# Performance work log

Measured on AMD Instinct MI355X. Metric: run time of the kernel, lower is better.

Reference implementation:

```python
import jax, jax.numpy as jnp
import numpy as np

B, N, D = 32, 20, 64          # graph pairs, max node set size, node state dim
NODE_F, EDGE_F = 16, 8        # raw feature dims
E_PER, PROP = 40, 5           # edges per graph, propagation steps
NC2 = N * (N - 1) // 2        # 190
TEMP, ITERS = 0.1, 20         # sinkhorn temperature / iterations
SRC, DST = np.triu_indices(N, 1)   # source_list / destination_list (len NC2)


def _lin(k, fin, fout):
    return jax.random.normal(k, (fin, fout), dtype=jnp.float32) / np.sqrt(fin).astype(np.float32)


def setup_inputs():
    key = jax.random.key(0)
    ks = jax.random.split(key, 24)
    tn, te = 2 * B * N, 2 * B * E_PER
    gid = jnp.repeat(jnp.arange(2 * B), E_PER)   # edges stay within their graph
    inp = {
        'node_features': jax.random.normal(ks[0], (tn, NODE_F), jnp.float32),
        'edge_features': jax.random.normal(ks[1], (te, EDGE_F), jnp.float32),
        'query_adj': (jax.random.uniform(ks[2], (B, N, N)) < 0.3).astype(jnp.float32),
        'corpus_adj': (jax.random.uniform(ks[3], (B, N, N)) < 0.3).astype(jnp.float32),
        'from_idx': jax.random.randint(ks[4], (te,), 0, N) + gid * N,
        'to_idx': jax.random.randint(ks[5], (te,), 0, N) + gid * N,
    }
    # GraphEncoder
    inp['Wn'] = _lin(ks[6], NODE_F, D); inp['bn'] = jnp.zeros(D)
    inp['We'] = _lin(ks[7], EDGE_F, D); inp['be'] = jnp.zeros(D)
    # GraphPropLayer: message net (in 3D) and node-update net (in 2D)
    inp['Wm1'] = _lin(ks[8], 3 * D, D); inp['bm1'] = jnp.zeros(D)
    inp['Wm2'] = _lin(ks[9], D, D);     inp['bm2'] = jnp.zeros(D)
    inp['Wu1'] = _lin(ks[10], 2 * D, D); inp['bu1'] = jnp.zeros(D)
    inp['Wu2'] = _lin(ks[11], D, D);     inp['bu2'] = jnp.zeros(D)
    # node_sinkhorn_feature_layers: Linear(D,N) -> ReLU -> Linear(N,N)
    inp['Ws1'] = _lin(ks[12], D, N); inp['bs1'] = jnp.zeros(N)
    inp['Ws2'] = _lin(ks[13], N, N); inp['bs2'] = jnp.zeros(N)
    # lrl_network: Linear(2D+1, D) -> ReLU -> Linear(D, D)
    inp['Wl1'] = _lin(ks[14], 2 * D + 1, D); inp['bl1'] = jnp.zeros(D)
    inp['Wl2'] = _lin(ks[15], D, D);         inp['bl2'] = jnp.zeros(D)
    return inp


def _mlp2(x, W1, b1, W2, b2):
    return jax.nn.relu(x @ W1 + b1) @ W2 + b2


def _sinkhorn(log_alpha):
    la = log_alpha / TEMP
    for _ in range(ITERS):
        la = la - jax.nn.logsumexp(la, axis=2, keepdims=True)
        la = la - jax.nn.logsumexp(la, axis=1, keepdims=True)
    return jnp.exp(la)


def _nc2_edge_emb(H, adj, Wl1, bl1, Wl2, bl2):
    s, d = H[:, SRC], H[:, DST]          # [B, NC2, D]
    e = adj[:, SRC, DST][..., None]      # [B, NC2, 1]
    fwd = _mlp2(jnp.concatenate([s, d, e], -1), Wl1, bl1, Wl2, bl2)
    bwd = _mlp2(jnp.concatenate([d, s, e], -1), Wl1, bl1, Wl2, bl2)
    return fwd + bwd


def reference(node_features, edge_features, query_adj, corpus_adj, from_idx, to_idx,
              Wn, bn, We, be, Wm1, bm1, Wm2, bm2, Wu1, bu1, Wu2, bu2,
              Ws1, bs1, Ws2, bs2, Wl1, bl1, Wl2, bl2):
    # encoder
    h = node_features @ Wn + bn
    e = edge_features @ We + be
    # GMN-style gather -> MLP -> scatter propagation
    for _ in range(PROP):
        msg = _mlp2(jnp.concatenate([h[from_idx], h[to_idx], e], -1), Wm1, bm1, Wm2, bm2)
        agg = jax.ops.segment_sum(msg, to_idx, num_segments=2 * B * N)
        h = _mlp2(jnp.concatenate([h, agg], -1), Wu1, bu1, Wu2, bu2)
    # split_and_stack (all graphs have exactly N nodes): query even, corpus odd
    H = h.reshape(2 * B, N, D)
    Hq, Hc = H[0::2], H[1::2]
    # node Sinkhorn over L1 cdist of transformed features
    Tq = _mlp2(Hq, Ws1, bs1, Ws2, bs2)
    Tc = _mlp2(Hc, Ws1, bs1, Ws2, bs2)
    cost = jnp.abs(Tq[:, :, None, :] - Tc[:, None, :, :]).sum(-1)   # [B, N, N]
    P = _sinkhorn(-cost)                                            # node transport plan
    qe = _nc2_edge_emb(Hq, query_adj, Wl1, bl1, Wl2, bl2)           # [B, NC2, D]
    ce = _nc2_edge_emb(Hc, corpus_adj, Wl1, bl1, Wl2, bl2)
    # 4-way gather-multiply edge scores: [B, NC2, NC2]
    straight = P[:, SRC[:, None], SRC[None, :]] * P[:, DST[:, None], DST[None, :]]
    cross = P[:, SRC[:, None], DST[None, :]] * P[:, DST[:, None], SRC[None, :]]
    esi = jnp.maximum(straight, cross)                              # use_max=True
    eplan = _sinkhorn(jnp.log(esi + 1e-6))                          # use_second_sinkhorn_log
    # use_m_ms_edge=True: pairwise asymmetric L1 alignment distance
    diff = qe[:, :, None, :] - ce[:, None, :, :]                    # [B, NC2, NC2, D]
    dist = (eplan * (jax.nn.relu(diff).sum(-1) + jax.nn.relu(-diff).sum(-1))).sum((-1, -2))
    return dist                                                      # [B]
```

## Files before the change

kernel.cpp:

```cpp
#include <hip/hip_runtime.h>
#include <math.h>

#define B_     32
#define N_     20
#define D_     64
#define NODE_F 16
#define EDGE_F 8
#define E_PER  40
#define PROP   5
#define NC2    190
#define ITERS  20
#define INV_TEMP 10.0f
#define TN (2*B_*N_)
#define TE (2*B_*E_PER)
#define NG (2*B_)

struct PairTab { int s[NC2]; int d[NC2]; };
constexpr PairTab make_pairs() {
    PairTab t{};
    int idx = 0;
    for (int i = 0; i < N_; ++i)
        for (int j = i + 1; j < N_; ++j) { t.s[idx] = i; t.d[idx] = j; ++idx; }
    return t;
}
__device__ constexpr PairTab PAIRS = make_pairs();

__device__ __forceinline__ float rlane(float x, int k) {
#if __has_builtin(__builtin_amdgcn_readlane)
    return __int_as_float(__builtin_amdgcn_readlane(__float_as_int(x), k));
#else
    return __shfl(x, k, 64);
#endif
}

template<int CTRL>
__device__ __forceinline__ float dppmov(float x) {
    return __int_as_float(__builtin_amdgcn_update_dpp(
        0, __float_as_int(x), CTRL, 0xf, 0xf, false));
}
__device__ __forceinline__ float rowsum16(float x) {
    x += dppmov<0x121>(x);
    x += dppmov<0x122>(x);
    x += dppmov<0x124>(x);
    x += dppmov<0x128>(x);
    return x;
}
__device__ __forceinline__ float rowmax16(float x) {
    x = fmaxf(x, dppmov<0x121>(x));
    x = fmaxf(x, dppmov<0x122>(x));
    x = fmaxf(x, dppmov<0x124>(x));
    x = fmaxf(x, dppmov<0x128>(x));
    return x;
}
__device__ __forceinline__ float nrcp(float x) {
    float r = __builtin_amdgcn_rcpf(x);
    r = r * fmaf(-x, r, 2.0f);
    return r;
}

__global__ __launch_bounds__(256) void k_encode(
    const float* __restrict__ nf, const float* __restrict__ ef,
    const float* __restrict__ Wn, const float* __restrict__ bn,
    const float* __restrict__ We, const float* __restrict__ be,
    float* __restrict__ h, float* __restrict__ eemb, float* __restrict__ agg)
{
    int gid = blockIdx.x * 256 + threadIdx.x;
    int f = gid & 63, r = gid >> 6;
    if (r < TN) {
        float acc = bn[f];
#pragma unroll
        for (int k = 0; k < NODE_F; ++k) acc += nf[r * NODE_F + k] * Wn[k * D_ + f];
        h[r * D_ + f] = acc;
        agg[r * D_ + f] = 0.f;
    } else if (r < TN + TE) {
        int r2 = r - TN;
        float acc = be[f];
#pragma unroll
        for (int k = 0; k < EDGE_F; ++k) acc += ef[r2 * EDGE_F + k] * We[k * D_ + f];
        eemb[r2 * D_ + f] = acc;
    }
}

#define EPW 4
__global__ __launch_bounds__(256) void k_msg(
    const float* __restrict__ h, const float* __restrict__ eemb,
    const int* __restrict__ fidx, const int* __restrict__ tidx,
    const float* __restrict__ Wm1, const float* __restrict__ bm1,
    const float* __restrict__ Wm2, const float* __restrict__ bm2,
    float* __restrict__ agg)
{
    int wid = (blockIdx.x * 256 + threadIdx.x) >> 6;
    int f = threadIdx.x & 63;
    int ebase = wid * EPW;
    float xf[EPW], xt[EPW], xe[EPW];
    int to[EPW];
#pragma unroll
    for (int s = 0; s < EPW; ++s) {
        int e = ebase + s;
        int fr = fidx[e]; to[s] = tidx[e];
        xf[s] = h[fr * D_ + f];
        xt[s] = h[to[s] * D_ + f];
        xe[s] = eemb[e * D_ + f];
    }
    float b1 = bm1[f];
    float acc[EPW];
#pragma unroll
    for (int s = 0; s < EPW; ++s) acc[s] = b1;
#pragma unroll 4
    for (int k = 0; k < D_; ++k) {
        float w0 = Wm1[k * D_ + f];
        float w1 = Wm1[(D_ + k) * D_ + f];
        float w2 = Wm1[(2 * D_ + k) * D_ + f];
#pragma unroll
        for (int s = 0; s < EPW; ++s)
            acc[s] += rlane(xf[s], k) * w0 + rlane(xt[s], k) * w1 + rlane(xe[s], k) * w2;
    }
    float b2 = bm2[f];
    float out[EPW];
#pragma unroll
    for (int s = 0; s < EPW; ++s) { acc[s] = fmaxf(acc[s], 0.f); out[s] = b2; }
#pragma unroll 4
    for (int k = 0; k < D_; ++k) {
        float w = Wm2[k * D_ + f];
#pragma unroll
        for (int s = 0; s < EPW; ++s) out[s] += rlane(acc[s], k) * w;
    }
#pragma unroll
    for (int s = 0; s < EPW; ++s) atomicAdd(&agg[to[s] * D_ + f], out[s]);
}

#define NPW 2
__global__ __launch_bounds__(256) void k_update(
    float* __restrict__ h, float* __restrict__ agg,
    const float* __restrict__ Wu1, const float* __restrict__ bu1,
    const float* __restrict__ Wu2, const float* __restrict__ bu2)
{
    int wid = (blockIdx.x * 256 + threadIdx.x) >> 6;
    int f = threadIdx.x & 63;
    int nbase = wid * NPW;
    float xh[NPW], xa[NPW];
#pragma unroll
    for (int s = 0; s < NPW; ++s) {
        xh[s] = h[(nbase + s) * D_ + f];
        xa[s] = agg[(nbase + s) * D_ + f];
    }
    float b1 = bu1[f];
    float acc[NPW];
#pragma unroll
    for (int s = 0; s < NPW; ++s) acc[s] = b1;
#pragma unroll 4
    for (int k = 0; k < D_; ++k) {
        float w0 = Wu1[k * D_ + f];
        float w1 = Wu1[(D_ + k) * D_ + f];
#pragma unroll
        for (int s = 0; s < NPW; ++s)
            acc[s] += rlane(xh[s], k) * w0 + rlane(xa[s], k) * w1;
    }
    float b2 = bu2[f];
    float out[NPW];
#pragma unroll
    for (int s = 0; s < NPW; ++s) { acc[s] = fmaxf(acc[s], 0.f); out[s] = b2; }
#pragma unroll 4
    for (int k = 0; k < D_; ++k) {
        float w = Wu2[k * D_ + f];
#pragma unroll
        for (int s = 0; s < NPW; ++s) out[s] += rlane(acc[s], k) * w;
    }
#pragma unroll
    for (int s = 0; s < NPW; ++s) {
        h[(nbase + s) * D_ + f] = out[s];
        agg[(nbase + s) * D_ + f] = 0.f;
    }
}

#define PPW 4
__global__ __launch_bounds__(256) void k_edge(
    const float* __restrict__ h,
    const float* __restrict__ qadj, const float* __restrict__ cadj,
    const float* __restrict__ Wl1, const float* __restrict__ bl1,
    const float* __restrict__ Wl2, const float* __restrict__ bl2,
    float* __restrict__ emb)
{
    int wid = (blockIdx.x * 256 + threadIdx.x) >> 6;
    int f = threadIdx.x & 63;
    int base = wid * PPW;
    float sv[PPW], dv[PPW], av[PPW];
#pragma unroll
    for (int s = 0; s < PPW; ++s) {
        int slot = base + s;
        int g = slot / NC2, p = slot - g * NC2;
        int sp = PAIRS.s[p], dp = PAIRS.d[p];
        sv[s] = h[(g * N_ + sp) * D_ + f];
        dv[s] = h[(g * N_ + dp) * D_ + f];
        const float* adj = (g & 1) ? cadj : qadj;
        av[s] = adj[(g >> 1) * N_ * N_ + sp * N_ + dp];
    }
    float b1 = bl1[f];
    float w128 = Wl1[128 * D_ + f];
    float aF[PPW], aB[PPW];
#pragma unroll
    for (int s = 0; s < PPW; ++s) { float t0 = b1 + av[s] * w128; aF[s] = t0; aB[s] = t0; }
#pragma unroll 2
    for (int k = 0; k < D_; ++k) {
        float w0 = Wl1[k * D_ + f];
        float w1 = Wl1[(D_ + k) * D_ + f];
#pragma unroll
        for (int s = 0; s < PPW; ++s) {
            float a = rlane(sv[s], k), c = rlane(dv[s], k);
            aF[s] += a * w0 + c * w1;
            aB[s] += c * w0 + a * w1;
        }
    }
    float b2 = 2.f * bl2[f];
    float hs[PPW], out[PPW];
#pragma unroll
    for (int s = 0; s < PPW; ++s) {
        hs[s] = fmaxf(aF[s], 0.f) + fmaxf(aB[s], 0.f);
        out[s] = b2;
    }
#pragma unroll 4
    for (int k = 0; k < D_; ++k) {
        float w = Wl2[k * D_ + f];
#pragma unroll
        for (int s = 0; s < PPW; ++s) out[s] += rlane(hs[s], k) * w;
    }
#pragma unroll
    for (int s = 0; s < PPW; ++s) emb[(size_t)(base + s) * D_ + f] = out[s];
}

__global__ __launch_bounds__(1024) void k_simsink(
    const float* __restrict__ h,
    const float* __restrict__ Ws1, const float* __restrict__ bs1,
    const float* __restrict__ Ws2, const float* __restrict__ bs2,
    float* __restrict__ eplan, float* __restrict__ dout)
{
    __shared__ float sH[2][N_][D_];
    __shared__ float sA[2][N_][N_];
    __shared__ float sT[2][N_][N_];
    __shared__ float sLa[N_][N_];
    __shared__ float sU20[N_], sV20[N_];
    __shared__ float sP[N_][N_];
    __shared__ float colbuf[64][200];
    __shared__ float sInvC[192];
    __shared__ short sQs[192], sQd[192];
    int b = blockIdx.x, t = threadIdx.x;

    for (int idx = t; idx < 2 * N_ * D_; idx += 1024) {
        int s = idx / (N_ * D_), rem = idx % (N_ * D_), i = rem / D_, f = rem % D_;
        sH[s][i][f] = h[((2 * b + s) * N_ + i) * D_ + f];
    }
    __syncthreads();
    for (int idx = t; idx < 2 * N_ * N_; idx += 1024) {
        int s = idx / (N_ * N_), rem = idx % (N_ * N_), i = rem / N_, k = rem % N_;
        float a = bs1[k];
        for (int ff = 0; ff < D_; ++ff) a += sH[s][i][ff] * Ws1[ff * N_ + k];
        sA[s][i][k] = fmaxf(a, 0.f);
    }
    __syncthreads();
    for (int idx = t; idx < 2 * N_ * N_; idx += 1024) {
        int s = idx / (N_ * N_), rem = idx % (N_ * N_), i = rem / N_, k = rem % N_;
        float a = bs2[k];
        for (int j = 0; j < N_; ++j) a += sA[s][i][j] * Ws2[j * N_ + k];
        sT[s][i][k] = a;
    }
    __syncthreads();
    for (int idx = t; idx < N_ * N_; idx += 1024) {
        int i = idx / N_, j = idx % N_;
        float c = 0.f;
        for (int k = 0; k < N_; ++k) c += fabsf(sT[0][i][k] - sT[1][j][k]);
        sLa[i][j] = -c * INV_TEMP;
    }
    if (t < N_) sV20[t] = 0.f;
    __syncthreads();
    for (int it = 0; it < ITERS; ++it) {
        if (t < N_) {
            float m = -1e30f;
            for (int q = 0; q < N_; ++q) m = fmaxf(m, sLa[t][q] - sV20[q]);
            float ss = 0.f;
            for (int q = 0; q < N_; ++q) ss += __expf(sLa[t][q] - sV20[q] - m);
            sU20[t] = m + __logf(ss);
        }
        __syncthreads();
        if (t < N_) {
            float m = -1e30f;
            for (int p = 0; p < N_; ++p) m = fmaxf(m, sLa[p][t] - sU20[p]);
            float ss = 0.f;
            for (int p = 0; p < N_; ++p) ss += __expf(sLa[p][t] - sU20[p] - m);
            sV20[t] = m + __logf(ss);
        }
        __syncthreads();
    }
    if (t < N_ * N_) {
        int i = t / N_, j = t % N_;
        sP[i][j] = __expf(sLa[i][j] - sU20[i] - sV20[j]);
    }
    if (t < 192) {
        int tt = t < NC2 ? t : NC2 - 1;
        sQs[t] = (short)PAIRS.s[tt];
        sQd[t] = (short)PAIRS.d[tt];
    }
    if (t == 0) dout[b] = 0.f;
    __syncthreads();

    int w = t >> 6, l = t & 63, g = l >> 4, l16 = l & 15;
    int rslot = w * 4 + g;

    int sp[3], dp[3];
    bool pv[3];
#pragma unroll
    for (int i = 0; i < 3; ++i) {
        int p = rslot + 64 * i;
        pv[i] = (p < NC2);
        int pp = pv[i] ? p : 0;
        sp[i] = sQs[pp]; dp[i] = sQd[pp];
    }
    int sq[12], dq[12];
    bool qv[12];
#pragma unroll
    for (int j = 0; j < 12; ++j) {
        int q = l16 + 16 * j;
        qv[j] = (q < NC2);
        int qq = qv[j] ? q : 0;
        sq[j] = sQs[qq]; dq[j] = sQd[qq];
    }

    float E[3][12];
#pragma unroll
    for (int i = 0; i < 3; ++i) {
        float mi = 1e-30f;
#pragma unroll
        for (int j = 0; j < 12; ++j) {
            float x = 0.f;
            if (pv[i] && qv[j]) {
                float st = sP[sp[i]][sq[j]] * sP[dp[i]][dq[j]];
                float cr = sP[sp[i]][dq[j]] * sP[dp[i]][sq[j]];
                x = fmaxf(st, cr) + 1e-6f;
            }
            E[i][j] = x;
            mi = fmaxf(mi, x);
        }
        mi = rowmax16(mi);
        float invm = nrcp(mi);
#pragma unroll
        for (int j = 0; j < 12; ++j) {
            float r = E[i][j] * invm;
            float r2 = r * r, r4 = r2 * r2, r8 = r4 * r4;
            E[i][j] = r8 * r2;
        }
    }

    float invS[3];
    for (int it = 0; it < ITERS; ++it) {
#pragma unroll
        for (int i = 0; i < 3; ++i) {
            float s01 = E[i][0] + E[i][1], s23 = E[i][2] + E[i][3];
            float s45 = E[i][4] + E[i][5], s67 = E[i][6] + E[i][7];
            float s89 = E[i][8] + E[i][9], sab = E[i][10] + E[i][11];
            float S = ((s01 + s23) + (s45 + s67)) + (s89 + sab);
            S = rowsum16(S);
            invS[i] = nrcp(fmaxf(S, 1e-30f));
        }
#pragma unroll
        for (int j = 0; j < 12; ++j) {
            float pc = E[0][j] * invS[0];
            pc = fmaf(E[1][j], invS[1], pc);
            pc = fmaf(E[2][j], invS[2], pc);
            colbuf[rslot][l16 + 16 * j] = pc;
        }
        __syncthreads();
        if (t < 192) {
            float a0 = 0.f, a1 = 0.f, a2 = 0.f, a3 = 0.f;
#pragma unroll
            for (int s = 0; s < 16; ++s) {
                a0 += colbuf[4 * s + 0][t];
                a1 += colbuf[4 * s + 1][t];
                a2 += colbuf[4 * s + 2][t];
                a3 += colbuf[4 * s + 3][t];
            }
            float c = (a0 + a1) + (a2 + a3);
            sInvC[t] = nrcp(fmaxf(c, 1e-30f));
        }
        __syncthreads();
        float ic[12];
#pragma unroll
        for (int j = 0; j < 12; ++j) ic[j] = sInvC[l16 + 16 * j];
#pragma unroll
        for (int i = 0; i < 3; ++i) {
#pragma unroll
            for (int j = 0; j < 12; ++j) {
                float tmp = E[i][j] * invS[i];
                E[i][j] = tmp * ic[j];
            }
        }
    }

    float* ep = eplan + (size_t)b * NC2 * NC2;
#pragma unroll
    for (int i = 0; i < 3; ++i) {
        if (pv[i]) {
            int p = rslot + 64 * i;
            float* row = ep + (size_t)p * NC2;
#pragma unroll
            for (int j = 0; j < 12; ++j) {
                if (qv[j]) row[l16 + 16 * j] = E[i][j];
            }
        }
    }
}

__global__ __launch_bounds__(256) void k_dist(
    const float* __restrict__ emb, const float* __restrict__ eplan, float* __restrict__ dout)
{
    int b = blockIdx.x, c = blockIdx.y;
    int w = threadIdx.x >> 6, l = threadIdx.x & 63;
    const float* qe = emb + (size_t)(2 * b) * NC2 * D_;
    const float* ce = emb + (size_t)(2 * b + 1) * NC2 * D_;
    const float* W = eplan + (size_t)b * NC2 * NC2;
    float acc = 0.f;
    int pbase = c * 16 + w * 4;
    for (int i = 0; i < 4; ++i) {
        int p = pbase + i;
        if (p >= NC2) break;
        float qv = qe[(size_t)p * D_ + l];
        const float* wrow = W + (size_t)p * NC2;
        for (int q = 0; q < NC2; ++q)
            acc += wrow[q] * fabsf(qv - ce[(size_t)q * D_ + l]);
    }
#pragma unroll
    for (int off = 32; off; off >>= 1) acc += __shfl_xor(acc, off);
    if (l == 0) atomicAdd(&dout[b], acc);
}

extern "C" void kernel_launch(void* const* d_in, const int* in_sizes, int n_in,
                              void* d_out, int out_size, void* d_ws, size_t ws_size,
                              hipStream_t stream)
{
    const float* nf   = (const float*)d_in[0];
    const float* ef   = (const float*)d_in[1];
    const float* qadj = (const float*)d_in[2];
    const float* cadj = (const float*)d_in[3];
    const int*   fidx = (const int*)d_in[4];
    const int*   tidx = (const int*)d_in[5];
    const float* Wn  = (const float*)d_in[6];  const float* bn  = (const float*)d_in[7];
    const float* We  = (const float*)d_in[8];  const float* be  = (const float*)d_in[9];
    const float* Wm1 = (const float*)d_in[10]; const float* bm1 = (const float*)d_in[11];
    const float* Wm2 = (const float*)d_in[12]; const float* bm2 = (const float*)d_in[13];
    const float* Wu1 = (const float*)d_in[14]; const float* bu1 = (const float*)d_in[15];
    const float* Wu2 = (const float*)d_in[16]; const float* bu2 = (const float*)d_in[17];
    const float* Ws1 = (const float*)d_in[18]; const float* bs1 = (const float*)d_in[19];
    const float* Ws2 = (const float*)d_in[20]; const float* bs2 = (const float*)d_in[21];
    const float* Wl1 = (const float*)d_in[22]; const float* bl1 = (const float*)d_in[23];
    const float* Wl2 = (const float*)d_in[24]; const float* bl2 = (const float*)d_in[25];

    float* ws    = (float*)d_ws;
    float* h     = ws;
    float* agg   = h    + (size_t)TN * D_;
    float* eemb  = agg  + (size_t)TN * D_;
    float* emb   = eemb + (size_t)TE * D_;
    float* eplan = emb  + (size_t)NG * NC2 * D_;
    float* dout  = (float*)d_out;

    k_encode<<<(TN + TE) * D_ / 256, 256, 0, stream>>>(nf, ef, Wn, bn, We, be, h, eemb, agg);
    for (int s = 0; s < PROP; ++s) {
        k_msg<<<TE / EPW / 4, 256, 0, stream>>>(h, eemb, fidx, tidx, Wm1, bm1, Wm2, bm2, agg);
        k_update<<<TN / NPW / 4, 256, 0, stream>>>(h, agg, Wu1, bu1, Wu2, bu2);
    }
    k_simsink<<<B_, 1024, 0, stream>>>(h, Ws1, bs1, Ws2, bs2, eplan, dout);
    k_edge<<<NG * NC2 / PPW / 4, 256, 0, stream>>>(h, qadj, cadj, Wl1, bl1, Wl2, bl2, emb);
    k_dist<<<dim3(B_, 12), 256, 0, stream>>>(emb, eplan, dout);
}
```

Before: 315.0 us.

## Fuse encoder, propagation, sinkhorn and edge embedding into one per-pair megakernel

Replaces the encode, five msg/update rounds, node/edge sinkhorn and edge-embedding kernels with a single 1024-thread block per graph pair. Node states, edge embeddings and aggregates live in shared memory, so the intermediate global round-trips and roughly a dozen launches go away. The node sinkhorn now runs on one wavefront using shuffles. The edge sinkhorn's first iteration is done in log domain instead of the max-normalised power trick. The cost is that only 32 blocks run all the propagation and edge-MLP work, which leaves most of the GPU idle during those phases.

```diff
diff --git a/kernel.cpp b/kernel.cpp
--- a/kernel.cpp
+++ b/kernel.cpp
@@ -26,30 +26,21 @@
 __device__ constexpr PairTab PAIRS = make_pairs();
 
 __device__ __forceinline__ float rlane(float x, int k) {
-#if __has_builtin(__builtin_amdgcn_readlane)
     return __int_as_float(__builtin_amdgcn_readlane(__float_as_int(x), k));
-#else
-    return __shfl(x, k, 64);
-#endif
-}
-
+}
 template<int CTRL>
 __device__ __forceinline__ float dppmov(float x) {
     return __int_as_float(__builtin_amdgcn_update_dpp(
         0, __float_as_int(x), CTRL, 0xf, 0xf, false));
 }
 __device__ __forceinline__ float rowsum16(float x) {
-    x += dppmov<0x121>(x);
-    x += dppmov<0x122>(x);
-    x += dppmov<0x124>(x);
-    x += dppmov<0x128>(x);
+    x += dppmov<0x121>(x); x += dppmov<0x122>(x);
+    x += dppmov<0x124>(x); x += dppmov<0x128>(x);
     return x;
 }
 __device__ __forceinline__ float rowmax16(float x) {
-    x = fmaxf(x, dppmov<0x121>(x));
-    x = fmaxf(x, dppmov<0x122>(x));
-    x = fmaxf(x, dppmov<0x124>(x));
-    x = fmaxf(x, dppmov<0x128>(x));
+    x = fmaxf(x, dppmov<0x121>(x)); x = fmaxf(x, dppmov<0x122>(x));
+    x = fmaxf(x, dppmov<0x124>(x)); x = fmaxf(x, dppmov<0x128>(x));
     return x;
 }
 __device__ __forceinline__ float nrcp(float x) {
@@ -58,351 +49,406 @@
     return r;
 }
 
-__global__ __launch_bounds__(256) void k_encode(
+__global__ __launch_bounds__(1024) void k_mega(
     const float* __restrict__ nf, const float* __restrict__ ef,
+    const float* __restrict__ qadj, const float* __restrict__ cadj,
+    const int* __restrict__ fidx, const int* __restrict__ tidx,
     const float* __restrict__ Wn, const float* __restrict__ bn,
     const float* __restrict__ We, const float* __restrict__ be,
-    float* __restrict__ h, float* __restrict__ eemb, float* __restrict__ agg)
-{
-    int gid = blockIdx.x * 256 + threadIdx.x;
-    int f = gid & 63, r = gid >> 6;
-    if (r < TN) {
-        float acc = bn[f];
-#pragma unroll
-        for (int k = 0; k < NODE_F; ++k) acc += nf[r * NODE_F + k] * Wn[k * D_ + f];
-        h[r * D_ + f] = acc;
-        agg[r * D_ + f] = 0.f;
-    } else if (r < TN + TE) {
-        int r2 = r - TN;
-        float acc = be[f];
-#pragma unroll
-        for (int k = 0; k < EDGE_F; ++k) acc += ef[r2 * EDGE_F + k] * We[k * D_ + f];
-        eemb[r2 * D_ + f] = acc;
-    }
-}
-
-#define EPW 4
-__global__ __launch_bounds__(256) void k_msg(
-    const float* __restrict__ h, const float* __restrict__ eemb,
-    const int* __restrict__ fidx, const int* __restrict__ tidx,
     const float* __restrict__ Wm1, const float* __restrict__ bm1,
     const float* __restrict__ Wm2, const float* __restrict__ bm2,
-    float* __restrict__ agg)
-{
-    int wid = (blockIdx.x * 256 + threadIdx.x) >> 6;
-    int f = threadIdx.x & 63;
-    int ebase = wid * EPW;
-    float xf[EPW], xt[EPW], xe[EPW];
-    int to[EPW];
-#pragma unroll
-    for (int s = 0; s < EPW; ++s) {
-        int e = ebase + s;
-        int fr = fidx[e]; to[s] = tidx[e];
-        xf[s] = h[fr * D_ + f];
-        xt[s] = h[to[s] * D_ + f];
-        xe[s] = eemb[e * D_ + f];
-    }
-    float b1 = bm1[f];
-    float acc[EPW];
-#pragma unroll
-    for (int s = 0; s < EPW; ++s) acc[s] = b1;
-#pragma unroll 4
-    for (int k = 0; k < D_; ++k) {
-        float w0 = Wm1[k * D_ + f];
-        float w1 = Wm1[(D_ + k) * D_ + f];
-        float w2 = Wm1[(2 * D_ + k) * D_ + f];
-#pragma unroll
-        for (int s = 0; s < EPW; ++s)
-            acc[s] += rlane(xf[s], k) * w0 + rlane(xt[s], k) * w1 + rlane(xe[s], k) * w2;
-    }
-    float b2 = bm2[f];
-    float out[EPW];
-#pragma unroll
-    for (int s = 0; s < EPW; ++s) { acc[s] = fmaxf(acc[s], 0.f); out[s] = b2; }
-#pragma unroll 4
-    for (int k = 0; k < D_; ++k) {
-        float w = Wm2[k * D_ + f];
-#pragma unroll
-        for (int s = 0; s < EPW; ++s) out[s] += rlane(acc[s], k) * w;
-    }
-#pragma unroll
-    for (int s = 0; s < EPW; ++s) atomicAdd(&agg[to[s] * D_ + f], out[s]);
-}
-
-#define NPW 2
-__global__ __launch_bounds__(256) void k_update(
-    float* __restrict__ h, float* __restrict__ agg,
     const float* __restrict__ Wu1, const float* __restrict__ bu1,
-    const float* __restrict__ Wu2, const float* __restrict__ bu2)
-{
-    int wid = (blockIdx.x * 256 + threadIdx.x) >> 6;
-    int f = threadIdx.x & 63;
-    int nbase = wid * NPW;
-    float xh[NPW], xa[NPW];
-#pragma unroll
-    for (int s = 0; s < NPW; ++s) {
-        xh[s] = h[(nbase + s) * D_ + f];
-        xa[s] = agg[(nbase + s) * D_ + f];
-    }
-    float b1 = bu1[f];
-    float acc[NPW];
-#pragma unroll
-    for (int s = 0; s < NPW; ++s) acc[s] = b1;
-#pragma unroll 4
-    for (int k = 0; k < D_; ++k) {
-        float w0 = Wu1[k * D_ + f];
-        float w1 = Wu1[(D_ + k) * D_ + f];
-#pragma unroll
-        for (int s = 0; s < NPW; ++s)
-            acc[s] += rlane(xh[s], k) * w0 + rlane(xa[s], k) * w1;
-    }
-    float b2 = bu2[f];
-    float out[NPW];
-#pragma unroll
-    for (int s = 0; s < NPW; ++s) { acc[s] = fmaxf(acc[s], 0.f); out[s] = b2; }
-#pragma unroll 4
-    for (int k = 0; k < D_; ++k) {
-        float w = Wu2[k * D_ + f];
-#pragma unroll
-        for (int s = 0; s < NPW; ++s) out[s] += rlane(acc[s], k) * w;
-    }
-#pragma unroll
-    for (int s = 0; s < NPW; ++s) {
-        h[(nbase + s) * D_ + f] = out[s];
-        agg[(nbase + s) * D_ + f] = 0.f;
-    }
-}
-
-#define PPW 4
-__global__ __launch_bounds__(256) void k_edge(
-    const float* __restrict__ h,
-    const float* __restrict__ qadj, const float* __restrict__ cadj,
+    const float* __restrict__ Wu2, const float* __restrict__ bu2,
+    const float* __restrict__ Ws1, const float* __restrict__ bs1,
+    const float* __restrict__ Ws2, const float* __restrict__ bs2,
     const float* __restrict__ Wl1, const float* __restrict__ bl1,
     const float* __restrict__ Wl2, const float* __restrict__ bl2,
-    float* __restrict__ emb)
+    float* __restrict__ emb, float* __restrict__ eplan, float* __restrict__ dout)
 {
-    int wid = (blockIdx.x * 256 + threadIdx.x) >> 6;
-    int f = threadIdx.x & 63;
-    int base = wid * PPW;
-    float sv[PPW], dv[PPW], av[PPW];
-#pragma unroll
-    for (int s = 0; s < PPW; ++s) {
-        int slot = base + s;
-        int g = slot / NC2, p = slot - g * NC2;
-        int sp = PAIRS.s[p], dp = PAIRS.d[p];
-        sv[s] = h[(g * N_ + sp) * D_ + f];
-        dv[s] = h[(g * N_ + dp) * D_ + f];
-        const float* adj = (g & 1) ? cadj : qadj;
-        av[s] = adj[(g >> 1) * N_ * N_ + sp * N_ + dp];
-    }
-    float b1 = bl1[f];
-    float w128 = Wl1[128 * D_ + f];
-    float aF[PPW], aB[PPW];
-#pragma unroll
-    for (int s = 0; s < PPW; ++s) { float t0 = b1 + av[s] * w128; aF[s] = t0; aB[s] = t0; }
-#pragma unroll 2
-    for (int k = 0; k < D_; ++k) {
-        float w0 = Wl1[k * D_ + f];
-        float w1 = Wl1[(D_ + k) * D_ + f];
-#pragma unroll
-        for (int s = 0; s < PPW; ++s) {
-            float a = rlane(sv[s], k), c = rlane(dv[s], k);
-            aF[s] += a * w0 + c * w1;
-            aB[s] += c * w0 + a * w1;
-        }
-    }
-    float b2 = 2.f * bl2[f];
-    float hs[PPW], out[PPW];
-#pragma unroll
-    for (int s = 0; s < PPW; ++s) {
-        hs[s] = fmaxf(aF[s], 0.f) + fmaxf(aB[s], 0.f);
-        out[s] = b2;
-    }
-#pragma unroll 4
-    for (int k = 0; k < D_; ++k) {
-        float w = Wl2[k * D_ + f];
-#pragma unroll
-        for (int s = 0; s < PPW; ++s) out[s] += rlane(hs[s], k) * w;
-    }
-#pragma unroll
-    for (int s = 0; s < PPW; ++s) emb[(size_t)(base + s) * D_ + f] = out[s];
-}
-
-__global__ __launch_bounds__(1024) void k_simsink(
-    const float* __restrict__ h,
-    const float* __restrict__ Ws1, const float* __restrict__ bs1,
-    const float* __restrict__ Ws2, const float* __restrict__ bs2,
-    float* __restrict__ eplan, float* __restrict__ dout)
-{
-    __shared__ float sH[2][N_][D_];
-    __shared__ float sA[2][N_][N_];
-    __shared__ float sT[2][N_][N_];
-    __shared__ float sLa[N_][N_];
-    __shared__ float sU20[N_], sV20[N_];
+    __shared__ float sh_h[40][64];
+    __shared__ short sFr[80], sTo[80];
+    __shared__ short sQs[192], sQd[192];
     __shared__ float sP[N_][N_];
-    __shared__ float colbuf[64][200];
-    __shared__ float sInvC[192];
-    __shared__ short sQs[192], sQd[192];
-    int b = blockIdx.x, t = threadIdx.x;
-
-    for (int idx = t; idx < 2 * N_ * D_; idx += 1024) {
-        int s = idx / (N_ * D_), rem = idx % (N_ * D_), i = rem / D_, f = rem % D_;
-        sH[s][i][f] = h[((2 * b + s) * N_ + i) * D_ + f];
-    }
-    __syncthreads();
-    for (int idx = t; idx < 2 * N_ * N_; idx += 1024) {
-        int s = idx / (N_ * N_), rem = idx % (N_ * N_), i = rem / N_, k = rem % N_;
-        float a = bs1[k];
-        for (int ff = 0; ff < D_; ++ff) a += sH[s][i][ff] * Ws1[ff * N_ + k];
-        sA[s][i][k] = fmaxf(a, 0.f);
-    }
-    __syncthreads();
-    for (int idx = t; idx < 2 * N_ * N_; idx += 1024) {
-        int s = idx / (N_ * N_), rem = idx % (N_ * N_), i = rem / N_, k = rem % N_;
-        float a = bs2[k];
-        for (int j = 0; j < N_; ++j) a += sA[s][i][j] * Ws2[j * N_ + k];
-        sT[s][i][k] = a;
-    }
-    __syncthreads();
-    for (int idx = t; idx < N_ * N_; idx += 1024) {
-        int i = idx / N_, j = idx % N_;
-        float c = 0.f;
-        for (int k = 0; k < N_; ++k) c += fabsf(sT[0][i][k] - sT[1][j][k]);
-        sLa[i][j] = -c * INV_TEMP;
-    }
-    if (t < N_) sV20[t] = 0.f;
-    __syncthreads();
-    for (int it = 0; it < ITERS; ++it) {
-        if (t < N_) {
-            float m = -1e30f;
-            for (int q = 0; q < N_; ++q) m = fmaxf(m, sLa[t][q] - sV20[q]);
-            float ss = 0.f;
-            for (int q = 0; q < N_; ++q) ss += __expf(sLa[t][q] - sV20[q] - m);
-            sU20[t] = m + __logf(ss);
-        }
-        __syncthreads();
-        if (t < N_) {
-            float m = -1e30f;
-            for (int p = 0; p < N_; ++p) m = fmaxf(m, sLa[p][t] - sU20[p]);
-            float ss = 0.f;
-            for (int p = 0; p < N_; ++p) ss += __expf(sLa[p][t] - sU20[p] - m);
-            sV20[t] = m + __logf(ss);
-        }
-        __syncthreads();
-    }
-    if (t < N_ * N_) {
-        int i = t / N_, j = t % N_;
-        sP[i][j] = __expf(sLa[i][j] - sU20[i] - sV20[j]);
+    __shared__ float sVbuf[192];
+    __shared__ float region[12416];
+    float* eemb = region;
+    float* agg  = region + 80 * 64;
+    float* sT   = region;
+    float* sLa  = region + 800;
+    float* colbuf = region;
+
+    int b = blockIdx.x, t = threadIdx.x, w = t >> 6, l = t & 63;
+
+    if (t < 80) {
+        sFr[t] = (short)(fidx[b * 80 + t] - b * 40);
+        sTo[t] = (short)(tidx[b * 80 + t] - b * 40);
     }
     if (t < 192) {
         int tt = t < NC2 ? t : NC2 - 1;
-        sQs[t] = (short)PAIRS.s[tt];
-        sQd[t] = (short)PAIRS.d[tt];
+        sQs[t] = (short)PAIRS.s[tt]; sQd[t] = (short)PAIRS.d[tt];
     }
     if (t == 0) dout[b] = 0.f;
+#pragma unroll
+    for (int s = 0; s < 3; ++s) {
+        int r = w + 16 * s;
+        if (r < 40) {
+            float acc = bn[l];
+#pragma unroll
+            for (int k = 0; k < NODE_F; ++k) acc += nf[(b * 40 + r) * NODE_F + k] * Wn[k * 64 + l];
+            sh_h[r][l] = acc;
+        }
+    }
+#pragma unroll
+    for (int s = 0; s < 5; ++s) {
+        int e = w * 5 + s;
+        float acc = be[l];
+#pragma unroll
+        for (int k = 0; k < EDGE_F; ++k) acc += ef[(b * 80 + e) * EDGE_F + k] * We[k * 64 + l];
+        eemb[e * 64 + l] = acc;
+    }
+    for (int idx = t; idx < 2560; idx += 1024) agg[idx] = 0.f;
     __syncthreads();
 
-    int w = t >> 6, l = t & 63, g = l >> 4, l16 = l & 15;
-    int rslot = w * 4 + g;
-
-    int sp[3], dp[3];
-    bool pv[3];
-#pragma unroll
-    for (int i = 0; i < 3; ++i) {
-        int p = rslot + 64 * i;
-        pv[i] = (p < NC2);
-        int pp = pv[i] ? p : 0;
-        sp[i] = sQs[pp]; dp[i] = sQd[pp];
-    }
-    int sq[12], dq[12];
-    bool qv[12];
-#pragma unroll
-    for (int j = 0; j < 12; ++j) {
-        int q = l16 + 16 * j;
-        qv[j] = (q < NC2);
-        int qq = qv[j] ? q : 0;
-        sq[j] = sQs[qq]; dq[j] = sQd[qq];
-    }
-
-    float E[3][12];
-#pragma unroll
-    for (int i = 0; i < 3; ++i) {
-        float mi = 1e-30f;
+    for (int step = 0; step < PROP; ++step) {
+        int eb = w * 5;
+        float xf[5], xt[5], xe[5]; int dst[5];
+#pragma unroll
+        for (int s = 0; s < 5; ++s) {
+            int fr = sFr[eb + s]; dst[s] = sTo[eb + s];
+            xf[s] = sh_h[fr][l];
+            xt[s] = sh_h[dst[s]][l];
+            xe[s] = eemb[(eb + s) * 64 + l];
+        }
+        float b1 = bm1[l];
+        float acc[5];
+#pragma unroll
+        for (int s = 0; s < 5; ++s) acc[s] = b1;
+#pragma unroll 4
+        for (int k = 0; k < 64; ++k) {
+            float w0 = Wm1[k * 64 + l];
+            float w1 = Wm1[(64 + k) * 64 + l];
+            float w2 = Wm1[(128 + k) * 64 + l];
+#pragma unroll
+            for (int s = 0; s < 5; ++s)
+                acc[s] += rlane(xf[s], k) * w0 + rlane(xt[s], k) * w1 + rlane(xe[s], k) * w2;
+        }
+        float b2 = bm2[l];
+        float out[5];
+#pragma unroll
+        for (int s = 0; s < 5; ++s) { acc[s] = fmaxf(acc[s], 0.f); out[s] = b2; }
+#pragma unroll 4
+        for (int k = 0; k < 64; ++k) {
+            float ww = Wm2[k * 64 + l];
+#pragma unroll
+            for (int s = 0; s < 5; ++s) out[s] += rlane(acc[s], k) * ww;
+        }
+#pragma unroll
+        for (int s = 0; s < 5; ++s) atomicAdd(&agg[dst[s] * 64 + l], out[s]);
+        __syncthreads();
+
+        float xh[3], xa[3];
+        bool nv[3] = {true, true, (w < 8)};
+#pragma unroll
+        for (int s = 0; s < 3; ++s) {
+            int r = w + 16 * s;
+            if (nv[s]) { xh[s] = sh_h[r][l]; xa[s] = agg[r * 64 + l]; }
+            else { xh[s] = 0.f; xa[s] = 0.f; }
+        }
+        float c1 = bu1[l];
+        float a2[3];
+#pragma unroll
+        for (int s = 0; s < 3; ++s) a2[s] = c1;
+#pragma unroll 4
+        for (int k = 0; k < 64; ++k) {
+            float wa = Wu1[k * 64 + l];
+            float wb = Wu1[(64 + k) * 64 + l];
+#pragma unroll
+            for (int s = 0; s < 3; ++s)
+                a2[s] += rlane(xh[s], k) * wa + rlane(xa[s], k) * wb;
+        }
+        float c2 = bu2[l];
+        float o2[3];
+#pragma unroll
+        for (int s = 0; s < 3; ++s) { a2[s] = fmaxf(a2[s], 0.f); o2[s] = c2; }
+#pragma unroll 4
+        for (int k = 0; k < 64; ++k) {
+            float ww = Wu2[k * 64 + l];
+#pragma unroll
+            for (int s = 0; s < 3; ++s) o2[s] += rlane(a2[s], k) * ww;
+        }
+#pragma unroll
+        for (int s = 0; s < 3; ++s) {
+            int r = w + 16 * s;
+            if (nv[s]) { sh_h[r][l] = o2[s]; agg[r * 64 + l] = 0.f; }
+        }
+        __syncthreads();
+    }
+
+    {
+        int lk = (l < 20) ? l : 0;
+#pragma unroll
+        for (int s = 0; s < 3; ++s) {
+            int r = w + 16 * s;
+            if (r < 40) {
+                float hv = sh_h[r][l];
+                float a = bs1[lk];
+#pragma unroll 4
+                for (int ff = 0; ff < 64; ++ff) a += rlane(hv, ff) * Ws1[ff * 20 + lk];
+                a = fmaxf(a, 0.f);
+                float t2 = bs2[lk];
+#pragma unroll
+                for (int j = 0; j < 20; ++j) t2 += rlane(a, j) * Ws2[j * 20 + lk];
+                if (l < 20) sT[(r >= 20) * 400 + (r % 20) * 20 + l] = t2;
+            }
+        }
+    }
+    __syncthreads();
+    if (t < 400) {
+        int i = t / 20, j = t % 20;
+        float c = 0.f;
+#pragma unroll
+        for (int k = 0; k < 20; ++k) c += fabsf(sT[i * 20 + k] - sT[400 + j * 20 + k]);
+        sLa[i * 20 + j] = -c * INV_TEMP;
+    }
+    __syncthreads();
+
+    if (w == 0) {
+        int q = l & 31, r2 = l >> 5;
+        bool qok = (q < 20);
+        float A20[10], u10[10];
+#pragma unroll
+        for (int i = 0; i < 10; ++i) {
+            int r = 2 * i + r2;
+            A20[i] = qok ? sLa[r * 20 + q] : -1e30f;
+        }
+        float vq = 0.f;
+        for (int it = 0; it < ITERS; ++it) {
+#pragma unroll
+            for (int i = 0; i < 10; ++i) {
+                float x = A20[i] - vq;
+                float m = x;
+#pragma unroll
+                for (int off = 16; off; off >>= 1) m = fmaxf(m, __shfl_xor(m, off));
+                float s = __expf(x - m);
+#pragma unroll
+                for (int off = 16; off; off >>= 1) s += __shfl_xor(s, off);
+                u10[i] = m + __logf(s);
+            }
+            float pm = -1e30f;
+#pragma unroll
+            for (int i = 0; i < 10; ++i) pm = fmaxf(pm, A20[i] - u10[i]);
+            float ps = 0.f;
+#pragma unroll
+            for (int i = 0; i < 10; ++i) ps += __expf(A20[i] - u10[i] - pm);
+            float om = __shfl_xor(pm, 32), os = __shfl_xor(ps, 32);
+            float M = fmaxf(pm, om);
+            float S = ps * __expf(pm - M) + os * __expf(om - M);
+            vq = M + __logf(S);
+            if (!qok) vq = 0.f;
+        }
+#pragma unroll
+        for (int i = 0; i < 10; ++i) {
+            int r = 2 * i + r2;
+            if (qok) sP[r][q] = __expf(A20[i] - u10[i] - vq);
+        }
+    }
+    __syncthreads();
+
+    {
+        float b1 = bl1[l];
+        float w128 = Wl1[128 * 64 + l];
+        float b2 = 2.f * bl2[l];
+        for (int bs = 0; bs < 6; ++bs) {
+            int base = w * 24 + bs * 4;
+            float sv[4], dv[4], av[4]; bool val[4]; int gg[4], pp[4];
+#pragma unroll
+            for (int s = 0; s < 4; ++s) {
+                int pl = base + s;
+                val[s] = (pl < 380);
+                int plc = val[s] ? pl : 0;
+                gg[s] = (plc >= 190) ? 1 : 0;
+                pp[s] = plc - gg[s] * 190;
+                int sp = sQs[pp[s]], dp = sQd[pp[s]];
+                sv[s] = sh_h[gg[s] * 20 + sp][l];
+                dv[s] = sh_h[gg[s] * 20 + dp][l];
+                const float* adj = gg[s] ? cadj : qadj;
+                av[s] = adj[b * 400 + sp * 20 + dp];
+            }
+            float aF[4], aB[4];
+#pragma unroll
+            for (int s = 0; s < 4; ++s) { float t0 = b1 + av[s] * w128; aF[s] = t0; aB[s] = t0; }
+#pragma unroll 2
+            for (int k = 0; k < 64; ++k) {
+                float w0 = Wl1[k * 64 + l];
+                float w1 = Wl1[(64 + k) * 64 + l];
+#pragma unroll
+                for (int s = 0; s < 4; ++s) {
+                    float a = rlane(sv[s], k), c = rlane(dv[s], k);
+                    aF[s] += a * w0 + c * w1;
+                    aB[s] += c * w0 + a * w1;
+                }
+            }
+            float hs[4], out[4];
+#pragma unroll
+            for (int s = 0; s < 4; ++s) { hs[s] = fmaxf(aF[s], 0.f) + fmaxf(aB[s], 0.f); out[s] = b2; }
+#pragma unroll 4
+            for (int k = 0; k < 64; ++k) {
+                float ww = Wl2[k * 64 + l];
+#pragma unroll
+                for (int s = 0; s < 4; ++s) out[s] += rlane(hs[s], k) * ww;
+            }
+#pragma unroll
+            for (int s = 0; s < 4; ++s)
+                if (val[s]) emb[((size_t)(2 * b + gg[s]) * NC2 + pp[s]) * 64 + l] = out[s];
+        }
+    }
+    __syncthreads();
+
+    {
+        int g4 = l >> 4, l16 = l & 15;
+        int rslot = w * 4 + g4;
+
+        int sp[3], dp[3]; bool pv[3];
+#pragma unroll
+        for (int i = 0; i < 3; ++i) {
+            int p = rslot + 64 * i;
+            pv[i] = (p < NC2);
+            int pc = pv[i] ? p : 0;
+            sp[i] = sQs[pc]; dp[i] = sQd[pc];
+        }
+        int sq[12], dq[12]; bool qv[12];
 #pragma unroll
         for (int j = 0; j < 12; ++j) {
-            float x = 0.f;
-            if (pv[i] && qv[j]) {
-                float st = sP[sp[i]][sq[j]] * sP[dp[i]][dq[j]];
-                float cr = sP[sp[i]][dq[j]] * sP[dp[i]][sq[j]];
-                x = fmaxf(st, cr) + 1e-6f;
-            }
-            E[i][j] = x;
-            mi = fmaxf(mi, x);
-        }
-        mi = rowmax16(mi);
-        float invm = nrcp(mi);
+            int q = l16 + 16 * j;
+            qv[j] = (q < NC2);
+            int qc = qv[j] ? q : 0;
+            sq[j] = sQs[qc]; dq[j] = sQd[qc];
+        }
+
+        float A[3][12];
+#pragma unroll
+        for (int i = 0; i < 3; ++i)
+#pragma unroll
+            for (int j = 0; j < 12; ++j) {
+                if (pv[i] && qv[j]) {
+                    float st = sP[sp[i]][sq[j]] * sP[dp[i]][dq[j]];
+                    float cr = sP[sp[i]][dq[j]] * sP[dp[i]][sq[j]];
+                    A[i][j] = __logf(fmaxf(st, cr) + 1e-6f) * INV_TEMP;
+                } else A[i][j] = -1e30f;
+            }
+
+        float u[3];
+#pragma unroll
+        for (int i = 0; i < 3; ++i) {
+            float m = -1e30f;
+#pragma unroll
+            for (int j = 0; j < 12; ++j) m = fmaxf(m, A[i][j]);
+            m = rowmax16(m);
+            float s = 0.f;
+#pragma unroll
+            for (int j = 0; j < 12; ++j) s += __expf(A[i][j] - m);
+            s = rowsum16(s);
+            u[i] = m + __logf(s);
+            if (!pv[i]) u[i] = 0.f;
+        }
 #pragma unroll
         for (int j = 0; j < 12; ++j) {
-            float r = E[i][j] * invm;
-            float r2 = r * r, r4 = r2 * r2, r8 = r4 * r4;
-            E[i][j] = r8 * r2;
-        }
-    }
-
-    float invS[3];
-    for (int it = 0; it < ITERS; ++it) {
+            float pm = -1e30f;
+#pragma unroll
+            for (int i = 0; i < 3; ++i) if (pv[i]) pm = fmaxf(pm, A[i][j] - u[i]);
+            colbuf[rslot * 194 + l16 + 16 * j] = pm;
+        }
+        __syncthreads();
+        if (t < 192) {
+            float M = -1e30f;
+#pragma unroll
+            for (int s = 0; s < 64; ++s) M = fmaxf(M, colbuf[s * 194 + t]);
+            sVbuf[t] = M;
+        }
+        __syncthreads();
+        float Mj[12];
+#pragma unroll
+        for (int j = 0; j < 12; ++j) Mj[j] = sVbuf[l16 + 16 * j];
+#pragma unroll
+        for (int j = 0; j < 12; ++j) {
+            float ps = 0.f;
+#pragma unroll
+            for (int i = 0; i < 3; ++i) if (pv[i]) ps += __expf(A[i][j] - u[i] - Mj[j]);
+            colbuf[rslot * 194 + l16 + 16 * j] = ps;
+        }
+        __syncthreads();
+        if (t < 192) {
+            float S = 0.f;
+#pragma unroll
+            for (int s = 0; s < 64; ++s) S += colbuf[s * 194 + t];
+            sVbuf[t] = sVbuf[t] + __logf(fmaxf(S, 1e-37f));
+        }
+        __syncthreads();
+        float E[3][12];
+#pragma unroll
+        for (int j = 0; j < 12; ++j) Mj[j] = sVbuf[l16 + 16 * j];
+#pragma unroll
+        for (int i = 0; i < 3; ++i)
+#pragma unroll
+            for (int j = 0; j < 12; ++j) {
+                float e = __expf(A[i][j] - u[i] - Mj[j]);
+                E[i][j] = (pv[i] && qv[j]) ? e : 0.f;
+            }
+        __syncthreads();
+
+        float invS[3];
+        for (int it = 0; it < ITERS - 1; ++it) {
+#pragma unroll
+            for (int i = 0; i < 3; ++i) {
+                float s01 = E[i][0] + E[i][1], s23 = E[i][2] + E[i][3];
+                float s45 = E[i][4] + E[i][5], s67 = E[i][6] + E[i][7];
+                float s89 = E[i][8] + E[i][9], sab = E[i][10] + E[i][11];
+                float S = ((s01 + s23) + (s45 + s67)) + (s89 + sab);
+                S = rowsum16(S);
+                invS[i] = nrcp(fmaxf(S, 1e-30f));
+            }
+#pragma unroll
+            for (int j = 0; j < 12; ++j) {
+                float pc = E[0][j] * invS[0];
+                pc = fmaf(E[1][j], invS[1], pc);
+                pc = fmaf(E[2][j], invS[2], pc);
+                colbuf[rslot * 194 + l16 + 16 * j] = pc;
+            }
+            __syncthreads();
+            if (t < 192) {
+                float a0 = 0.f, a1 = 0.f, a2 = 0.f, a3 = 0.f;
+#pragma unroll
+                for (int s = 0; s < 16; ++s) {
+                    a0 += colbuf[(4 * s + 0) * 194 + t];
+                    a1 += colbuf[(4 * s + 1) * 194 + t];
+                    a2 += colbuf[(4 * s + 2) * 194 + t];
+                    a3 += colbuf[(4 * s + 3) * 194 + t];
+                }
+                float c = (a0 + a1) + (a2 + a3);
+                sVbuf[t] = nrcp(fmaxf(c, 1e-30f));
+            }
+            __syncthreads();
+            float ic[12];
+#pragma unroll
+            for (int j = 0; j < 12; ++j) ic[j] = sVbuf[l16 + 16 * j];
+#pragma unroll
+            for (int i = 0; i < 3; ++i)
+#pragma unroll
+                for (int j = 0; j < 12; ++j) {
+                    float tmp = E[i][j] * invS[i];
+                    E[i][j] = tmp * ic[j];
+                }
+        }
+
+        float* ep = eplan + (size_t)b * NC2 * NC2;
 #pragma unroll
         for (int i = 0; i < 3; ++i) {
-            float s01 = E[i][0] + E[i][1], s23 = E[i][2] + E[i][3];
-            float s45 = E[i][4] + E[i][5], s67 = E[i][6] + E[i][7];
-            float s89 = E[i][8] + E[i][9], sab = E[i][10] + E[i][11];
-            float S = ((s01 + s23) + (s45 + s67)) + (s89 + sab);
-            S = rowsum16(S);
-            invS[i] = nrcp(fmaxf(S, 1e-30f));
-        }
-#pragma unroll
-        for (int j = 0; j < 12; ++j) {
-            float pc = E[0][j] * invS[0];
-            pc = fmaf(E[1][j], invS[1], pc);
-            pc = fmaf(E[2][j], invS[2], pc);
-            colbuf[rslot][l16 + 16 * j] = pc;
-        }
-        __syncthreads();
-        if (t < 192) {
-            float a0 = 0.f, a1 = 0.f, a2 = 0.f, a3 = 0.f;
-#pragma unroll
-            for (int s = 0; s < 16; ++s) {
-                a0 += colbuf[4 * s + 0][t];
-                a1 += colbuf[4 * s + 1][t];
-                a2 += colbuf[4 * s + 2][t];
-                a3 += colbuf[4 * s + 3][t];
-            }
-            float c = (a0 + a1) + (a2 + a3);
-            sInvC[t] = nrcp(fmaxf(c, 1e-30f));
-        }
-        __syncthreads();
-        float ic[12];
-#pragma unroll
-        for (int j = 0; j < 12; ++j) ic[j] = sInvC[l16 + 16 * j];
-#pragma unroll
-        for (int i = 0; i < 3; ++i) {
-#pragma unroll
-            for (int j = 0; j < 12; ++j) {
-                float tmp = E[i][j] * invS[i];
-                E[i][j] = tmp * ic[j];
-            }
-        }
-    }
-
-    float* ep = eplan + (size_t)b * NC2 * NC2;
-#pragma unroll
-    for (int i = 0; i < 3; ++i) {
-        if (pv[i]) {
-            int p = rslot + 64 * i;
-            float* row = ep + (size_t)p * NC2;
-#pragma unroll
-            for (int j = 0; j < 12; ++j) {
-                if (qv[j]) row[l16 + 16 * j] = E[i][j];
+            if (pv[i]) {
+                int p = rslot + 64 * i;
+                float* row = ep + (size_t)p * NC2;
+#pragma unroll
+                for (int j = 0; j < 12; ++j)
+                    if (qv[j]) row[l16 + 16 * j] = E[i][j];
             }
         }
     }
@@ -453,19 +499,13 @@
     const float* Wl2 = (const float*)d_in[24]; const float* bl2 = (const float*)d_in[25];
 
     float* ws    = (float*)d_ws;
-    float* h     = ws;
-    float* agg   = h    + (size_t)TN * D_;
-    float* eemb  = agg  + (size_t)TN * D_;
-    float* emb   = eemb + (size_t)TE * D_;
-    float* eplan = emb  + (size_t)NG * NC2 * D_;
+    float* emb   = ws;
+    float* eplan = emb + (size_t)NG * NC2 * D_;
     float* dout  = (float*)d_out;
 
-    k_encode<<<(TN + TE) * D_ / 256, 256, 0, stream>>>(nf, ef, Wn, bn, We, be, h, eemb, agg);
-    for (int s = 0; s < PROP; ++s) {
-        k_msg<<<TE / EPW / 4, 256, 0, stream>>>(h, eemb, fidx, tidx, Wm1, bm1, Wm2, bm2, agg);
-        k_update<<<TN / NPW / 4, 256, 0, stream>>>(h, agg, Wu1, bu1, Wu2, bu2);
-    }
-    k_simsink<<<B_, 1024, 0, stream>>>(h, Ws1, bs1, Ws2, bs2, eplan, dout);
-    k_edge<<<NG * NC2 / PPW / 4, 256, 0, stream>>>(h, qadj, cadj, Wl1, bl1, Wl2, bl2, emb);
+    k_mega<<<B_, 1024, 0, stream>>>(nf, ef, qadj, cadj, fidx, tidx,
+                                    Wn, bn, We, be, Wm1, bm1, Wm2, bm2,
+                                    Wu1, bu1, Wu2, bu2, Ws1, bs1, Ws2, bs2,
+                                    Wl1, bl1, Wl2, bl2, emb, eplan, dout);
     k_dist<<<dim3(B_, 12), 256, 0, stream>>>(emb, eplan, dout);
 }
```

Measured after the change: 583.0 us. +85.1%, slower.
